# Performance work log

Measured on AMD Instinct MI355X. Metric: run time of the kernel, lower is better.

## Reference

```python
import jax, jax.numpy as jnp
import numpy as np

NUM_HEADS = 8
GROUPS = 32
EPS = 1e-5


def group_norm(x, gamma, beta):
    # x: (b, c, L)
    b, c, L = x.shape
    xg = x.reshape(b, GROUPS, c // GROUPS, L)
    mean = xg.mean(axis=(2, 3), keepdims=True)
    var = xg.var(axis=(2, 3), keepdims=True)
    xn = ((xg - mean) / jnp.sqrt(var + EPS)).reshape(b, c, L)
    return xn * gamma[None, :, None] + beta[None, :, None]


def setup_inputs() -> dict:
    key = jax.random.key(0)
    ks = jax.random.split(key, 8)
    b, c, h, w = 8, 512, 32, 32
    inner = c  # inner_channels == -1 -> channels
    x = jax.random.normal(ks[0], (b, c, h, w), dtype=jnp.float32)
    gamma = jnp.ones((c,), dtype=jnp.float32)
    beta = jnp.zeros((c,), dtype=jnp.float32)
    Wq = jax.random.normal(ks[1], (inner, c), dtype=jnp.float32) * 0.02
    bq = jnp.zeros((inner,), dtype=jnp.float32)
    Wkv = jax.random.normal(ks[2], (2 * inner, c), dtype=jnp.float32) * 0.02
    bkv = jnp.zeros((2 * inner,), dtype=jnp.float32)
    Wo = jax.random.normal(ks[3], (c, inner), dtype=jnp.float32) * 0.02
    bo = jnp.zeros((c,), dtype=jnp.float32)
    return {"x": x, "gamma": gamma, "beta": beta, "Wq": Wq, "bq": bq,
            "Wkv": Wkv, "bkv": bkv, "Wo": Wo, "bo": bo}


def reference(x, gamma, beta, Wq, bq, Wkv, bkv, Wo, bo):
    b, c = x.shape[:2]
    spatial = x.shape[2:]
    L = int(np.prod(spatial))
    inner = Wq.shape[0]
    dh = inner // NUM_HEADS
    scale = dh ** -0.5  # NOTE: applied to BOTH q and k, as in the source

    xr = x.reshape(b, c, L)
    hn = group_norm(xr, gamma, beta)          # norm(x); also serves as context

    # 1x1 Conv1d == channel matmul
    q = jnp.einsum('oc,bcl->bol', Wq, hn) + bq[None, :, None]
    kv = jnp.einsum('oc,bcl->bol', Wkv, hn) + bkv[None, :, None]
    k, v = jnp.split(kv, 2, axis=1)

    # (b, heads, dh, L)
    qh = (q * scale).reshape(b, NUM_HEADS, dh, L)
    kh = (k * scale).reshape(b, NUM_HEADS, dh, L)
    vh = v.reshape(b, NUM_HEADS, dh, L)

    dots = jnp.einsum('bhdt,bhds->bhts', qh, kh)
    attn = jax.nn.softmax(dots.astype(jnp.float32), axis=-1).astype(dots.dtype)
    out = jnp.einsum('bhts,bhds->bhdt', attn, vh)  # (b, heads, dh, L)

    out = out.reshape(b, inner, L)
    # output Linear over the channel dim
    out = jnp.einsum('oc,bcl->bol', Wo, out) + bo[None, :, None]
    return (xr + out).reshape(b, c, *spatial)
```

## Files before the change

### kernel.cpp

```cpp
#include <hip/hip_runtime.h>
#include <math.h>

#define B_ 8
#define C_ 512
#define L_ 1024
#define NH_ 8
#define DH_ 64
#define EPS 1e-5f
#define SCALE 0.125f
#define QSCALE (0.125f * 1.44269504088896f)

typedef __bf16 bf16x8 __attribute__((ext_vector_type(8)));
typedef __bf16 bf16x4 __attribute__((ext_vector_type(4)));
typedef float  f32x4  __attribute__((ext_vector_type(4)));
typedef float  f32x16 __attribute__((ext_vector_type(16)));

#define MFMA16(a, b, c) __builtin_amdgcn_mfma_f32_16x16x32_bf16((a), (b), (c), 0, 0, 0)
#define MFMA32(a, b, c) __builtin_amdgcn_mfma_f32_32x32x16_bf16((a), (b), (c), 0, 0, 0)

__device__ __forceinline__ void glds16(const __bf16* g, __bf16* l) {
    __builtin_amdgcn_global_load_lds((const __attribute__((address_space(1))) void*)(g),
                                     (__attribute__((address_space(3))) void*)(l),
                                     16, 0, 0);
}

__global__ __launch_bounds__(256)
void prep_kernel(const float* __restrict__ Wq, const float* __restrict__ Wkv,
                 const float* __restrict__ Wo, __bf16* __restrict__ dst,
                 const float* __restrict__ x, float* __restrict__ stats) {
    __shared__ float rs[256], rss[256];
    int bid = blockIdx.x, tid = threadIdx.x;
    if (bid < 1024) {
        int idx = bid * 256 + tid;
        float4 v;
        if (idx < 65536)        v = ((const float4*)Wq)[idx];
        else if (idx < 196608)  v = ((const float4*)Wkv)[idx - 65536];
        else                    v = ((const float4*)Wo)[idx - 196608];
        bf16x4 o;
        o[0] = (__bf16)v.x; o[1] = (__bf16)v.y; o[2] = (__bf16)v.z; o[3] = (__bf16)v.w;
        ((bf16x4*)dst)[idx] = o;
        return;
    }
    int bg = bid - 1024;
    size_t goff = (size_t)bg * 16 * L_;
    const float4* x4 = (const float4*)(x + goff);
    float s = 0.f, ss = 0.f;
    for (int i = tid; i < 4096; i += 256) {
        float4 v = x4[i];
        s  += v.x + v.y + v.z + v.w;
        ss += v.x * v.x + v.y * v.y + v.z * v.z + v.w * v.w;
    }
    rs[tid] = s; rss[tid] = ss;
    __syncthreads();
    for (int off = 128; off > 0; off >>= 1) {
        if (tid < off) { rs[tid] += rs[tid + off]; rss[tid] += rss[tid + off]; }
        __syncthreads();
    }
    if (tid == 0) {
        const float inv_n = 1.f / 16384.f;
        float mean = rs[0] * inv_n;
        float var  = rss[0] * inv_n - mean * mean;
        stats[bg * 2]     = mean;
        stats[bg * 2 + 1] = rsqrtf(var + EPS);
    }
}

__global__ __launch_bounds__(256)
void gn_apply_kernel(const float* __restrict__ x, const float* __restrict__ gamma,
                     const float* __restrict__ beta, const float* __restrict__ stats,
                     __bf16* __restrict__ hnT) {
    __shared__ __bf16 T[32 * 520];
    const int lt = blockIdx.x, b = blockIdx.y;
    const int tid = threadIdx.x;
    const int l0 = lt * 32;
    const int cbase = tid >> 3, fl = tid & 7;
#pragma unroll
    for (int p = 0; p < 16; ++p) {
        int cc = cbase + p * 32;
        float4 v = *(const float4*)&x[((size_t)b * C_ + cc) * L_ + l0 + fl * 4];
        int bg = b * 32 + (cc >> 4);
        float m = stats[bg * 2], rstd = stats[bg * 2 + 1];
        float ga = gamma[cc] * rstd, be = beta[cc];
        T[(fl * 4 + 0) * 520 + cc] = (__bf16)((v.x - m) * ga + be);
        T[(fl * 4 + 1) * 520 + cc] = (__bf16)((v.y - m) * ga + be);
        T[(fl * 4 + 2) * 520 + cc] = (__bf16)((v.z - m) * ga + be);
        T[(fl * 4 + 3) * 520 + cc] = (__bf16)((v.w - m) * ga + be);
    }
    __syncthreads();
    const int lrow = tid >> 6, cu = tid & 63;
#pragma unroll
    for (int pp = 0; pp < 8; ++pp) {
        int l = pp * 4 + lrow;
        bf16x8 r = *(const bf16x8*)&T[l * 520 + cu * 8];
        *(bf16x8*)&hnT[((size_t)b * L_ + l0 + l) * C_ + cu * 8] = r;
    }
}

__device__ __forceinline__
void gemm_mainloop(const __bf16* __restrict__ A, const __bf16* __restrict__ Bp,
                   __bf16* As, __bf16* Bs, f32x4 acc[4][4]) {
    const int tid = threadIdx.x;
    const int lane = tid & 63, w = tid >> 6;
    const int c = lane & 15, q = lane >> 4;
    const int wm = (w >> 1) * 64, wn = (w & 1) * 64;
    const int l8 = lane >> 3, kgsw = (lane & 7) ^ l8;

    for (int k0 = 0; k0 < 512; k0 += 64) {
#pragma unroll
        for (int i = 0; i < 4; ++i) {
            int chunk = w * 4 + i;
            int row = chunk * 8 + l8;
            glds16(A  + (size_t)row * 512 + k0 + kgsw * 8, &As[chunk * 512]);
            glds16(Bp + (size_t)row * 512 + k0 + kgsw * 8, &Bs[chunk * 512]);
        }
        __syncthreads();
#pragma unroll
        for (int ks = 0; ks < 2; ++ks) {
            const int koff = ((ks * 4 + q) ^ (c & 7)) * 8;
            bf16x8 af[4], bfr[4];
#pragma unroll
            for (int m = 0; m < 4; ++m)
                af[m] = *(const bf16x8*)&As[(wm + m * 16 + c) * 64 + koff];
#pragma unroll
            for (int n = 0; n < 4; ++n)
                bfr[n] = *(const bf16x8*)&Bs[(wn + n * 16 + c) * 64 + koff];
#pragma unroll
            for (int m = 0; m < 4; ++m)
#pragma unroll
                for (int n = 0; n < 4; ++n)
                    acc[m][n] = MFMA16(af[m], bfr[n], acc[m][n]);
        }
        __syncthreads();
    }
}

__global__ __launch_bounds__(256)
void qkv_kernel(const __bf16* __restrict__ Wq_bf, const __bf16* __restrict__ Wkv_bf,
                const __bf16* __restrict__ hnT,
                const float* __restrict__ bq, const float* __restrict__ bkv,
                __bf16* __restrict__ qT, __bf16* __restrict__ kT,
                __bf16* __restrict__ vv) {
    __shared__ __bf16 SMEM[128 * 64 * 2];
    __bf16* As = SMEM;
    __bf16* Bs = SMEM + 128 * 64;
    const int b = blockIdx.y;
    const int xx = blockIdx.x;
    const int sec = xx >> 5, t = xx & 31;
    const __bf16* hb = hnT + (size_t)b * L_ * C_;

    const __bf16 *A, *Bp;
    int m0, n0;
    if (sec < 2) {
        m0 = (t & 3) * 128; n0 = (t >> 2) * 128;
        A  = (sec == 0 ? Wq_bf : Wkv_bf) + (size_t)m0 * 512;
        Bp = hb + (size_t)n0 * 512;
    } else {
        m0 = (t >> 2) * 128; n0 = (t & 3) * 128;
        A  = hb + (size_t)m0 * 512;
        Bp = Wkv_bf + (size_t)(512 + n0) * 512;
    }

    f32x4 acc[4][4];
#pragma unroll
    for (int m = 0; m < 4; ++m)
#pragma unroll
        for (int n = 0; n < 4; ++n)
#pragma unroll
            for (int r = 0; r < 4; ++r) acc[m][n][r] = 0.f;

    gemm_mainloop(A, Bp, As, Bs, acc);

    const int tid = threadIdx.x, lane = tid & 63, w = tid >> 6;
    const int c = lane & 15, q = lane >> 4;
    const int wm = (w >> 1) * 64, wn = (w & 1) * 64;

    __bf16* T2 = SMEM;
    const float* bias = (sec == 0) ? bq : bkv;
    const float scl = (sec == 0) ? QSCALE : SCALE;
#pragma unroll
    for (int mt = 0; mt < 4; ++mt)
#pragma unroll
        for (int nt = 0; nt < 4; ++nt) {
            int n_loc = wn + nt * 16 + c;
            int u4 = (wm >> 2) + mt * 4 + q;
            int u4sw = u4 ^ ((n_loc & 7) << 1);
            bf16x4 ov;
            if (sec < 2) {
                int ob = m0 + wm + mt * 16 + q * 4;
#pragma unroll
                for (int r = 0; r < 4; ++r)
                    ov[r] = (__bf16)((acc[mt][nt][r] + bias[ob + r]) * scl);
            } else {
                float bi = bkv[512 + n0 + n_loc];
#pragma unroll
                for (int r = 0; r < 4; ++r)
                    ov[r] = (__bf16)(acc[mt][nt][r] + bi);
            }
            *(bf16x4*)&T2[n_loc * 128 + u4sw * 4] = ov;
        }
    __syncthreads();
#pragma unroll
    for (int p = 0; p < 8; ++p) {
        int rrow = p * 16 + (tid >> 4);
        int u16 = tid & 15;
        int u4p = (u16 * 2) ^ ((rrow & 7) << 1);
        bf16x8 val = *(const bf16x8*)&T2[rrow * 128 + u4p * 4];
        if (sec < 2) {
            int l = n0 + rrow;
            int og = m0 + u16 * 8;
            int hh = og >> 6, d0 = og & 63;
            __bf16* dstp = (sec == 0) ? qT : kT;
            *(bf16x8*)&dstp[((size_t)(b * NH_ + hh) * L_ + l) * DH_ + d0] = val;
        } else {
            int o = n0 + rrow;
            int lg = m0 + u16 * 8;
            *(bf16x8*)&vv[((size_t)b * C_ + o) * L_ + lg] = val;
        }
    }
}

__global__ __launch_bounds__(256, 2)
void attn_kernel(const __bf16* __restrict__ qT, const __bf16* __restrict__ kT,
                 const __bf16* __restrict__ vv, __bf16* __restrict__ aoT) {
    const int bid = blockIdx.x;
    const int wg = (bid & 7) * 64 + (bid >> 3);
    const int tt = wg & 7, h = (wg >> 3) & 7, b = wg >> 6;
    const int t0 = tt * 128;
    __shared__ __bf16 Qs[128 * 64];
    __shared__ __bf16 Ks[2][64 * 64];
    __shared__ __bf16 Vs[2][64 * 64];

    const int tid = threadIdx.x, lane = tid & 63, w = tid >> 6;
    const int l8 = lane >> 3, kg = (lane & 7) ^ l8;
    const int ln = lane & 31, hi = lane >> 5, r7 = ln & 7;

    const __bf16* qbase = qT + ((size_t)(b * NH_ + h) * L_ + t0) * DH_;
    const __bf16* kbase = kT + (size_t)(b * NH_ + h) * L_ * DH_;
    const __bf16* vbase = vv + (size_t)(b * C_ + h * DH_) * L_;

#pragma unroll
    for (int i = 0; i < 4; ++i) {
        int chunk = w * 4 + i;
        glds16(qbase + (size_t)(chunk * 8 + l8) * DH_ + kg * 8, &Qs[chunk * 512]);
    }
#pragma unroll
    for (int buf = 0; buf < 2; ++buf)
#pragma unroll
        for (int i = 0; i < 2; ++i) {
            int chunk = w * 2 + i, row = chunk * 8 + l8;
            glds16(kbase + (size_t)(buf * 64 + row) * DH_ + kg * 8, &Ks[buf][chunk * 512]);
            glds16(vbase + (size_t)row * L_ + buf * 64 + kg * 8, &Vs[buf][chunk * 512]);
        }
    asm volatile("s_waitcnt vmcnt(4)" ::: "memory");
    asm volatile("s_barrier" ::: "memory");

    f32x16 o_acc[2];
#pragma unroll
    for (int dt = 0; dt < 2; ++dt)
#pragma unroll
        for (int r = 0; r < 16; ++r) o_acc[dt][r] = 0.f;
    float l_own = 0.f;

    const int qrow = w * 32 + ln;

    for (int it = 0; it < 16; ++it) {
        const __bf16* Kc = Ks[it & 1];
        const __bf16* Vc = Vs[it & 1];

        f32x16 sres[2];
#pragma unroll
        for (int mt = 0; mt < 2; ++mt)
#pragma unroll
            for (int r = 0; r < 16; ++r) sres[mt][r] = 0.f;
#pragma unroll
        for (int ks = 0; ks < 4; ++ks) {
            bf16x8 bQ = *(const bf16x8*)&Qs[qrow * 64 + ((ks * 2 + hi) ^ r7) * 8];
#pragma unroll
            for (int mt = 0; mt < 2; ++mt) {
                bf16x8 aK = *(const bf16x8*)&Kc[(mt * 32 + ln) * 64 + ((ks * 2 + hi) ^ r7) * 8];
                sres[mt] = MFMA32(aK, bQ, sres[mt]);
            }
        }

        bf16x8 frag[4];
#pragma unroll
        for (int mt = 0; mt < 2; ++mt) {
            float pv[16];
#pragma unroll
            for (int r = 0; r < 16; ++r) pv[r] = exp2f(sres[mt][r]);
            float s0a = (pv[0] + pv[1]) + (pv[2] + pv[3]);
            float s1a = (pv[4] + pv[5]) + (pv[6] + pv[7]);
            float s2a = (pv[8] + pv[9]) + (pv[10] + pv[11]);
            float s3a = (pv[12] + pv[13]) + (pv[14] + pv[15]);
            l_own += (s0a + s1a) + (s2a + s3a);
            unsigned int P[8];
#pragma unroll
            for (int j = 0; j < 8; ++j)
                asm("v_cvt_pk_bf16_f32 %0, %1, %2" : "=v"(P[j]) : "v"(pv[2 * j]), "v"(pv[2 * j + 1]));
            asm("v_permlane32_swap_b32 %0, %1" : "+v"(P[0]), "+v"(P[2]));
            asm("v_permlane32_swap_b32 %0, %1" : "+v"(P[1]), "+v"(P[3]));
            asm("v_permlane32_swap_b32 %0, %1" : "+v"(P[4]), "+v"(P[6]));
            asm("v_permlane32_swap_b32 %0, %1" : "+v"(P[5]), "+v"(P[7]));
            union FU { unsigned int u[4]; bf16x8 v; } fa, fb;
            fa.u[0] = P[0]; fa.u[1] = P[1]; fa.u[2] = P[2]; fa.u[3] = P[3];
            fb.u[0] = P[4]; fb.u[1] = P[5]; fb.u[2] = P[6]; fb.u[3] = P[7];
            frag[mt * 2 + 0] = fa.v;
            frag[mt * 2 + 1] = fb.v;
        }

#pragma unroll
        for (int ks2 = 0; ks2 < 4; ++ks2) {
#pragma unroll
            for (int dt = 0; dt < 2; ++dt) {
                bf16x8 aV = *(const bf16x8*)&Vc[(dt * 32 + ln) * 64 + ((ks2 * 2 + hi) ^ r7) * 8];
                o_acc[dt] = MFMA32(aV, frag[ks2], o_acc[dt]);
            }
        }

        asm volatile("s_barrier" ::: "memory");
        if (it < 14) {
            int s0n = (it + 2) * 64;
#pragma unroll
            for (int i = 0; i < 2; ++i) {
                int chunk = w * 2 + i, row = chunk * 8 + l8;
                glds16(kbase + (size_t)(s0n + row) * DH_ + kg * 8, &Ks[it & 1][chunk * 512]);
                glds16(vbase + (size_t)row * L_ + s0n + kg * 8, &Vs[it & 1][chunk * 512]);
            }
            asm volatile("s_waitcnt vmcnt(4)" ::: "memory");
        } else {
            asm volatile("s_waitcnt vmcnt(0)" ::: "memory");
        }
        asm volatile("s_barrier" ::: "memory");
    }

    float l_tot = l_own + __shfl_xor(l_own, 32);
    float linv = 1.f / l_tot;
    const int tg = t0 + w * 32 + ln;
    __bf16* aobase = aoT + ((size_t)b * L_ + tg) * C_ + h * DH_;
#pragma unroll
    for (int dt = 0; dt < 2; ++dt)
#pragma unroll
        for (int rq = 0; rq < 4; ++rq) {
            bf16x4 ov;
#pragma unroll
            for (int j = 0; j < 4; ++j) ov[j] = (__bf16)(o_acc[dt][rq * 4 + j] * linv);
            *(bf16x4*)&aobase[dt * 32 + rq * 8 + hi * 4] = ov;
        }
}

__global__ __launch_bounds__(256)
void proj_kernel(const __bf16* __restrict__ aoT, const __bf16* __restrict__ Wo_bf,
                 const float* __restrict__ bo, const float* __restrict__ x,
                 float* __restrict__ out) {
    __shared__ __bf16 As[128 * 64], Bs[128 * 64];
    const int b = blockIdx.y, t = blockIdx.x;
    const int m0 = (t >> 2) * 128;
    const int n0 = (t & 3) * 128;
    const __bf16* A  = aoT + (size_t)b * L_ * C_ + (size_t)m0 * 512;
    const __bf16* Bp = Wo_bf + (size_t)n0 * 512;

    f32x4 acc[4][4];
#pragma unroll
    for (int m = 0; m < 4; ++m)
#pragma unroll
        for (int n = 0; n < 4; ++n)
#pragma unroll
            for (int r = 0; r < 4; ++r) acc[m][n][r] = 0.f;

    gemm_mainloop(A, Bp, As, Bs, acc);

    const int tid = threadIdx.x, lane = tid & 63, w = tid >> 6;
    const int c = lane & 15, q = lane >> 4;
    const int wm = (w >> 1) * 64, wn = (w & 1) * 64;

#pragma unroll
    for (int mt = 0; mt < 4; ++mt)
#pragma unroll
        for (int nt = 0; nt < 4; ++nt) {
            int lb = m0 + wm + mt * 16 + q * 4;
            int o  = n0 + wn + nt * 16 + c;
            float bi = bo[o];
            size_t off = ((size_t)b * C_ + o) * L_ + lb;
            float4 xv = *(const float4*)&x[off];
            float4 rv;
            rv.x = acc[mt][nt][0] + bi + xv.x;
            rv.y = acc[mt][nt][1] + bi + xv.y;
            rv.z = acc[mt][nt][2] + bi + xv.z;
            rv.w = acc[mt][nt][3] + bi + xv.w;
            *(float4*)&out[off] = rv;
        }
}

extern "C" void kernel_launch(void* const* d_in, const int* in_sizes, int n_in,
                              void* d_out, int out_size, void* d_ws, size_t ws_size,
                              hipStream_t stream) {
    const float* x     = (const float*)d_in[0];
    const float* gamma = (const float*)d_in[1];
    const float* beta  = (const float*)d_in[2];
    const float* Wq    = (const float*)d_in[3];
    const float* bq    = (const float*)d_in[4];
    const float* Wkv   = (const float*)d_in[5];
    const float* bkv   = (const float*)d_in[6];
    const float* Wo    = (const float*)d_in[7];
    const float* bo    = (const float*)d_in[8];
    float* out = (float*)d_out;

    __bf16* wsb = (__bf16*)d_ws;
    __bf16* Wq_bf  = wsb;
    __bf16* Wkv_bf = wsb + 262144;
    __bf16* Wo_bf  = wsb + 786432;
    __bf16* hnT    = wsb + 1048576;
    __bf16* qT     = wsb + 5242880;
    __bf16* kT     = wsb + 9437184;
    __bf16* vv     = wsb + 13631488;
    __bf16* aoT    = wsb + 17825792;
    float*  stats  = (float*)(wsb + 22020096);

    prep_kernel<<<dim3(1280), 256, 0, stream>>>(Wq, Wkv, Wo, wsb, x, stats);
    gn_apply_kernel<<<dim3(32, B_), 256, 0, stream>>>(x, gamma, beta, stats, hnT);
    qkv_kernel<<<dim3(96, B_), 256, 0, stream>>>(Wq_bf, Wkv_bf, hnT, bq, bkv, qT, kT, vv);
    attn_kernel<<<dim3(512), 256, 0, stream>>>(qT, kT, vv, aoT);
    proj_kernel<<<dim3(32, B_), 256, 0, stream>>>(aoT, Wo_bf, bo, x, out);
}
```

Before: 166.5 us.

## Double-buffer GEMM mainloop, remap blocks across XCDs, raise MFMA priority in attention

The shared GEMM mainloop now uses two LDS buffers and prefetches the next K tile with async global-to-LDS loads while MFMAs run on the current tile, replacing the load-sync-compute-sync pattern. The qkv and proj launches become 1D grids with a block-id remap so that blocks of the same batch land on the same XCD, aiming for better L2 reuse of hnT/aoT. The attention kernel wraps its MFMA sections in s_setprio to favour matrix issue. Doubling LDS per block may reduce occupancy.

```diff
diff --git a/kernel.cpp b/kernel.cpp
--- a/kernel.cpp
+++ b/kernel.cpp
@@ -105,32 +105,52 @@
     const int wm = (w >> 1) * 64, wn = (w & 1) * 64;
     const int l8 = lane >> 3, kgsw = (lane & 7) ^ l8;
 
-    for (int k0 = 0; k0 < 512; k0 += 64) {
+#pragma unroll
+    for (int buf = 0; buf < 2; ++buf)
 #pragma unroll
         for (int i = 0; i < 4; ++i) {
             int chunk = w * 4 + i;
             int row = chunk * 8 + l8;
-            glds16(A  + (size_t)row * 512 + k0 + kgsw * 8, &As[chunk * 512]);
-            glds16(Bp + (size_t)row * 512 + k0 + kgsw * 8, &Bs[chunk * 512]);
-        }
-        __syncthreads();
+            glds16(A  + (size_t)row * 512 + buf * 64 + kgsw * 8, &As[buf * 8192 + chunk * 512]);
+            glds16(Bp + (size_t)row * 512 + buf * 64 + kgsw * 8, &Bs[buf * 8192 + chunk * 512]);
+        }
+    asm volatile("s_waitcnt vmcnt(8)" ::: "memory");
+    asm volatile("s_barrier" ::: "memory");
+
+    for (int it = 0; it < 8; ++it) {
+        const __bf16* Ac = As + (it & 1) * 8192;
+        const __bf16* Bc = Bs + (it & 1) * 8192;
 #pragma unroll
         for (int ks = 0; ks < 2; ++ks) {
             const int koff = ((ks * 4 + q) ^ (c & 7)) * 8;
             bf16x8 af[4], bfr[4];
 #pragma unroll
             for (int m = 0; m < 4; ++m)
-                af[m] = *(const bf16x8*)&As[(wm + m * 16 + c) * 64 + koff];
+                af[m] = *(const bf16x8*)&Ac[(wm + m * 16 + c) * 64 + koff];
 #pragma unroll
             for (int n = 0; n < 4; ++n)
-                bfr[n] = *(const bf16x8*)&Bs[(wn + n * 16 + c) * 64 + koff];
+                bfr[n] = *(const bf16x8*)&Bc[(wn + n * 16 + c) * 64 + koff];
 #pragma unroll
             for (int m = 0; m < 4; ++m)
 #pragma unroll
                 for (int n = 0; n < 4; ++n)
                     acc[m][n] = MFMA16(af[m], bfr[n], acc[m][n]);
         }
-        __syncthreads();
+        asm volatile("s_barrier" ::: "memory");
+        if (it < 6) {
+            int k0n = (it + 2) * 64;
+#pragma unroll
+            for (int i = 0; i < 4; ++i) {
+                int chunk = w * 4 + i;
+                int row = chunk * 8 + l8;
+                glds16(A  + (size_t)row * 512 + k0n + kgsw * 8, &As[(it & 1) * 8192 + chunk * 512]);
+                glds16(Bp + (size_t)row * 512 + k0n + kgsw * 8, &Bs[(it & 1) * 8192 + chunk * 512]);
+            }
+            asm volatile("s_waitcnt vmcnt(8)" ::: "memory");
+        } else {
+            asm volatile("s_waitcnt vmcnt(0)" ::: "memory");
+        }
+        asm volatile("s_barrier" ::: "memory");
     }
 }
 
@@ -140,11 +160,13 @@
                 const float* __restrict__ bq, const float* __restrict__ bkv,
                 __bf16* __restrict__ qT, __bf16* __restrict__ kT,
                 __bf16* __restrict__ vv) {
-    __shared__ __bf16 SMEM[128 * 64 * 2];
+    __shared__ __bf16 SMEM[128 * 64 * 4];
     __bf16* As = SMEM;
-    __bf16* Bs = SMEM + 128 * 64;
-    const int b = blockIdx.y;
-    const int xx = blockIdx.x;
+    __bf16* Bs = SMEM + 16384;
+    const int bid = blockIdx.x;
+    const int wgid = (bid & 7) * 96 + (bid >> 3);
+    const int b = wgid / 96;
+    const int xx = wgid % 96;
     const int sec = xx >> 5, t = xx & 31;
     const __bf16* hb = hnT + (size_t)b * L_ * C_;
 
@@ -272,6 +294,7 @@
         for (int mt = 0; mt < 2; ++mt)
 #pragma unroll
             for (int r = 0; r < 16; ++r) sres[mt][r] = 0.f;
+        __builtin_amdgcn_s_setprio(1);
 #pragma unroll
         for (int ks = 0; ks < 4; ++ks) {
             bf16x8 bQ = *(const bf16x8*)&Qs[qrow * 64 + ((ks * 2 + hi) ^ r7) * 8];
@@ -281,6 +304,7 @@
                 sres[mt] = MFMA32(aK, bQ, sres[mt]);
             }
         }
+        __builtin_amdgcn_s_setprio(0);
 
         bf16x8 frag[4];
 #pragma unroll
@@ -308,6 +332,7 @@
             frag[mt * 2 + 1] = fb.v;
         }
 
+        __builtin_amdgcn_s_setprio(1);
 #pragma unroll
         for (int ks2 = 0; ks2 < 4; ++ks2) {
 #pragma unroll
@@ -316,6 +341,7 @@
                 o_acc[dt] = MFMA32(aV, frag[ks2], o_acc[dt]);
             }
         }
+        __builtin_amdgcn_s_setprio(0);
 
         asm volatile("s_barrier" ::: "memory");
         if (it < 14) {
@@ -352,8 +378,10 @@
 void proj_kernel(const __bf16* __restrict__ aoT, const __bf16* __restrict__ Wo_bf,
                  const float* __restrict__ bo, const float* __restrict__ x,
                  float* __restrict__ out) {
-    __shared__ __bf16 As[128 * 64], Bs[128 * 64];
-    const int b = blockIdx.y, t = blockIdx.x;
+    __shared__ __bf16 As[2 * 8192], Bs[2 * 8192];
+    const int bid = blockIdx.x;
+    const int wgid = (bid & 7) * 32 + (bid >> 3);
+    const int b = wgid >> 5, t = wgid & 31;
     const int m0 = (t >> 2) * 128;
     const int n0 = (t & 3) * 128;
     const __bf16* A  = aoT + (size_t)b * L_ * C_ + (size_t)m0 * 512;
@@ -418,7 +446,7 @@
 
     prep_kernel<<<dim3(1280), 256, 0, stream>>>(Wq, Wkv, Wo, wsb, x, stats);
     gn_apply_kernel<<<dim3(32, B_), 256, 0, stream>>>(x, gamma, beta, stats, hnT);
-    qkv_kernel<<<dim3(96, B_), 256, 0, stream>>>(Wq_bf, Wkv_bf, hnT, bq, bkv, qT, kT, vv);
+    qkv_kernel<<<dim3(768), 256, 0, stream>>>(Wq_bf, Wkv_bf, hnT, bq, bkv, qT, kT, vv);
     attn_kernel<<<dim3(512), 256, 0, stream>>>(qT, kT, vv, aoT);
-    proj_kernel<<<dim3(32, B_), 256, 0, stream>>>(aoT, Wo_bf, bo, x, out);
-}
+    proj_kernel<<<dim3(256), 256, 0, stream>>>(aoT, Wo_bf, bo, x, out);
+}
```

Measured after the change: 160.8 us. -3.4%, faster.
